# Kernel tuning notes

Measured on AMD Instinct MI355X. Metric: run time of the kernel, lower is better.

The kernel has to match this reference:

```python
import jax, jax.numpy as jnp
import numpy as np

N_HEADS = 16
ROPE_THETA = 10000.0


def _rope(x):
    # x: (b, h, t, d). Interleaved-pair rotary embedding (lucidrains
    # rotary_embedding_torch convention: rotate_half on (d r) pairs, r=2).
    b, h, t, d = x.shape
    inv_freq = 1.0 / (ROPE_THETA ** (jnp.arange(0, d, 2, dtype=jnp.float32) / d))  # (d/2,)
    ang = jnp.arange(t, dtype=jnp.float32)[:, None] * inv_freq[None, :]            # (t, d/2)
    cos = jnp.cos(ang)
    sin = jnp.sin(ang)
    xp = x.reshape(b, h, t, d // 2, 2)
    x1, x2 = xp[..., 0], xp[..., 1]
    o1 = x1 * cos - x2 * sin
    o2 = x1 * sin + x2 * cos
    return jnp.stack([o1, o2], axis=-1).reshape(b, h, t, d)


def setup_inputs() -> dict:
    key = jax.random.key(0)
    k1, k2, k3 = jax.random.split(key, 3)
    B, T, C = 4, 2048, 1024
    x = jax.random.normal(k1, (B, T, C), dtype=jnp.float32)
    # torch nn.Linear weight layout: (out_features, in_features)
    w_attn = jax.random.normal(k2, (3 * C, C), dtype=jnp.float32) * (1.0 / np.sqrt(C))
    w_proj = jax.random.normal(k3, (C, C), dtype=jnp.float32) * (1.0 / np.sqrt(C))
    return {"x": x, "w_attn": w_attn, "w_proj": w_proj}


def reference(x, w_attn, w_proj):
    B, T, C = x.shape
    H = N_HEADS
    D = C // H
    # fused QKV projection: (b, t, 3C)
    qkv = jnp.einsum('btc,fc->btf', x, w_attn)
    # rearrange 'b t (r h d) -> r b h t d'
    qkv = qkv.reshape(B, T, 3, H, D).transpose(2, 0, 3, 1, 4)
    q, k, v = qkv[0], qkv[1], qkv[2]
    q = _rope(q)
    k = _rope(k)
    scale = 1.0 / np.sqrt(D).astype(np.float32)
    scores = jnp.einsum('bhqd,bhkd->bhqk', q, k) * scale
    attn = jax.nn.softmax(scores, axis=-1)
    y = jnp.einsum('bhqk,bhkd->bhqd', attn, v)       # (b, h, t, d)
    y = y.transpose(0, 2, 1, 3).reshape(B, T, C)     # 'b h t d -> b t (h d)'
    return jnp.einsum('btc,oc->bto', y, w_proj)
```

## Files before the change

kernel.cpp:

```cpp
#include <hip/hip_runtime.h>
#include <hip/hip_bf16.h>
#include <math.h>

typedef __bf16 bf16;
typedef float f32x4 __attribute__((ext_vector_type(4)));
typedef float f32x16 __attribute__((ext_vector_type(16)));
typedef bf16 bf16x8 __attribute__((ext_vector_type(8)));
typedef bf16 bf16x4 __attribute__((ext_vector_type(4)));
typedef unsigned int uint;
typedef uint uintx2 __attribute__((ext_vector_type(2)));

#define MFMA16(a, b, c) __builtin_amdgcn_mfma_f32_16x16x32_bf16(a, b, c, 0, 0, 0)
#define MFMA32(a, b, c) __builtin_amdgcn_mfma_f32_32x32x16_bf16(a, b, c, 0, 0, 0)

static constexpr int T_SEQ = 2048;
static constexpr int CDIM  = 1024;
static constexpr int NH    = 16;
static constexpr int DH    = 64;
static constexpr float FREQ_C = 0.20762050593045998f;
static constexpr float Q_SCALE = 0.18033688011112042f;

__device__ __forceinline__ float fexp2(float x) {
    return __builtin_amdgcn_exp2f(x);
}

__device__ __forceinline__ uint pack_bf16(float lo, float hi) {
    union { bf16 h[2]; uint u; } cv;
    cv.h[0] = (bf16)lo;
    cv.h[1] = (bf16)hi;
    return cv.u;
}

__device__ __forceinline__ void gld_lds16(const bf16* g, bf16* l) {
    __builtin_amdgcn_global_load_lds(
        (const __attribute__((address_space(1))) void*)g,
        (__attribute__((address_space(3))) void*)l, 16, 0, 0);
}

__device__ __forceinline__ void fast_sincos(float x, float* s, float* c) {
    const float INV2PI = 0.15915494309189535f;
    const float PI2_HI = 6.28125f;
    const float PI2_LO = 1.9353071795864769e-3f;
    const float n = rintf(x * INV2PI);
    float r = fmaf(-n, PI2_HI, x);
    r = fmaf(-n, PI2_LO, r);
    *s = __sinf(r);
    *c = __cosf(r);
}

__global__ __launch_bounds__(256)
void rope_table(float2* __restrict__ tab) {
    const int i = blockIdx.x * 256 + threadIdx.x;
    const int t = i >> 5, p = i & 31;
    const float ang = (float)t * exp2f(-2.0f * (float)p * FREQ_C);
    float s, c;
    fast_sincos(ang, &s, &c);
    tab[i] = make_float2(c, s);
}

__global__ __launch_bounds__(256)
void cvt_f32_bf16(const float* __restrict__ in, bf16* __restrict__ out, int n8) {
    const int i = blockIdx.x * 256 + threadIdx.x;
    if (i >= n8) return;
    const f32x4* p = (const f32x4*)(in + (size_t)i * 8);
    const f32x4 lo = p[0], hi = p[1];
    bf16x8 o;
    o[0] = (bf16)lo[0]; o[1] = (bf16)lo[1]; o[2] = (bf16)lo[2]; o[3] = (bf16)lo[3];
    o[4] = (bf16)hi[0]; o[5] = (bf16)hi[1]; o[6] = (bf16)hi[2]; o[7] = (bf16)hi[3];
    *(bf16x8*)(out + (size_t)i * 8) = o;
}

#define GEMM_CORE(Abase, Bbase, KDIM)                                            \
    f32x4 acc[4][4] = {};                                                        \
    for (int kk = 0; kk < (KDIM); kk += 64) {                                    \
        __syncthreads();                                                         \
        _Pragma("unroll")                                                        \
        for (int u = 0; u < 4; u++) {                                            \
            const int st = wave * 4 + u, mg = st >> 1, kg = st & 1;              \
            gld_lds16(Abase + (size_t)(mg * 16 + sm) * (KDIM) + kk + kg * 32 + sc * 8, \
                      &ash[st * 512]);                                           \
            gld_lds16(Bbase + (size_t)(mg * 16 + sm) * (KDIM) + kk + kg * 32 + sc * 8, \
                      &bsh[st * 512]);                                           \
        }                                                                        \
        __syncthreads();                                                         \
        _Pragma("unroll")                                                        \
        for (int kg = 0; kg < 2; kg++) {                                         \
            bf16x8 af[4], bfr[4];                                                \
            _Pragma("unroll")                                                    \
            for (int a = 0; a < 4; a++)                                          \
                af[a] = *(const bf16x8*)&ash[((wm * 4 + a) * 2 + kg) * 512 + lane * 8]; \
            _Pragma("unroll")                                                    \
            for (int b = 0; b < 4; b++)                                          \
                bfr[b] = *(const bf16x8*)&bsh[((wn * 4 + b) * 2 + kg) * 512 + lane * 8]; \
            _Pragma("unroll")                                                    \
            for (int a = 0; a < 4; a++)                                          \
                _Pragma("unroll")                                                \
                for (int b = 0; b < 4; b++)                                      \
                    acc[a][b] = MFMA16(af[a], bfr[b], acc[a][b]);                \
        }                                                                        \
    }

__global__ __launch_bounds__(256)
void gemm_qkv(const bf16* __restrict__ X, const bf16* __restrict__ W,
              bf16* __restrict__ Qo, bf16* __restrict__ Ko, bf16* __restrict__ Vt,
              const float2* __restrict__ tab) {
    __shared__ __align__(16) bf16 ash[16 * 512];
    __shared__ __align__(16) bf16 bsh[16 * 512];
    const int tid = threadIdx.x, lane = tid & 63, wave = tid >> 6;
    const int quad = lane >> 4, l16 = lane & 15;
    const int wm = wave >> 1, wn = wave & 1;
    const int bm = blockIdx.y, bn = blockIdx.x;
    const int sm = lane & 15, sc = lane >> 4;

    const bf16* Abase = X + (size_t)(bm * 128) * CDIM;
    const bf16* Bbase = W + (size_t)(bn * 128) * CDIM;
    GEMM_CORE(Abase, Bbase, CDIM)

    const int rr    = (bn * 128) >> 10;
    const int nsec  = (bn * 128) & 1023;
    const int batch = (bm * 128) >> 11;
    const int tb    = ((bm * 128) & 2047) + wm * 64;

    if (rr == 2) {
#pragma unroll
        for (int b = 0; b < 4; b++) {
            const int n = nsec + wn * 64 + b * 16 + l16;
            const int h = n >> 6, d = n & 63;
            bf16* vp = Vt + ((size_t)(batch * NH + h) * DH + d) * T_SEQ;
#pragma unroll
            for (int a = 0; a < 4; a++) {
                const int t0 = tb + a * 16 + quad * 4;
                bf16x4 pk4 = { (bf16)acc[a][b][0], (bf16)acc[a][b][1],
                               (bf16)acc[a][b][2], (bf16)acc[a][b][3] };
                *(bf16x4*)(vp + t0) = pk4;
            }
        }
    } else {
        bf16* Dst = (rr == 0) ? Qo : Ko;
        const float scale = (rr == 0) ? Q_SCALE : 1.0f;
#pragma unroll
        for (int b = 0; b < 4; b++) {
            const int n = nsec + wn * 64 + b * 16 + l16;
            const int h = n >> 6, d = n & 63;
            const int p = d >> 1, odd = d & 1;
            bf16* dp = Dst + (size_t)(batch * NH + h) * T_SEQ * DH + d;
#pragma unroll
            for (int a = 0; a < 4; a++) {
#pragma unroll
                for (int r = 0; r < 4; r++) {
                    const int t = tb + a * 16 + quad * 4 + r;
                    const float val = acc[a][b][r];
                    const float partner = __shfl_xor(val, 1);
                    const float2 cs = tab[t * 32 + p];
                    float o = odd ? (partner * cs.y + val * cs.x)
                                  : (val * cs.x - partner * cs.y);
                    dp[(size_t)t * DH] = (bf16)(o * scale);
                }
            }
        }
    }
}

__global__ __launch_bounds__(256)
void gemm_proj(const bf16* __restrict__ X, const bf16* __restrict__ W,
               float* __restrict__ Out) {
    __shared__ __align__(16) bf16 ash[16 * 512];
    __shared__ __align__(16) bf16 bsh[16 * 512];
    const int tid = threadIdx.x, lane = tid & 63, wave = tid >> 6;
    const int quad = lane >> 4, l16 = lane & 15;
    const int wm = wave >> 1, wn = wave & 1;
    const int bm = blockIdx.y, bn = blockIdx.x;
    const int sm = lane & 15, sc = lane >> 4;

    const bf16* Abase = X + (size_t)(bm * 128) * CDIM;
    const bf16* Bbase = W + (size_t)(bn * 128) * CDIM;
    GEMM_CORE(Abase, Bbase, CDIM)

#pragma unroll
    for (int b = 0; b < 4; b++) {
        const int n = bn * 128 + wn * 64 + b * 16 + l16;
#pragma unroll
        for (int a = 0; a < 4; a++) {
            const int m = bm * 128 + wm * 64 + a * 16 + quad * 4;
#pragma unroll
            for (int r = 0; r < 4; r++)
                Out[(size_t)(m + r) * CDIM + n] = acc[a][b][r];
        }
    }
}

__global__ __launch_bounds__(256)
void flash(const bf16* __restrict__ Q, const bf16* __restrict__ K,
           const bf16* __restrict__ Vt, bf16* __restrict__ Y) {
    __shared__ __align__(16) bf16 ksh[2][8 * 512];
    __shared__ __align__(16) bf16 vsh[2][8 * 512];
    const int tid = threadIdx.x, lane = tid & 63, wave = tid >> 6;
    const int l32 = lane & 31, hi = lane >> 5;
    const int id = blockIdx.x;
    const int bh = (id & 7) * 8 + ((id >> 3) & 7);
    const int qb = id >> 6;
    const size_t kbase = (size_t)bh * T_SEQ * DH;
    const size_t vbase = (size_t)bh * DH * T_SEQ;
    const int q0 = qb * 128 + wave * 32;

    bf16x8 bq[4];
    const bf16* qp = Q + kbase + (size_t)(q0 + l32) * DH + hi * 8;
#pragma unroll
    for (int c = 0; c < 4; c++) bq[c] = *(const bf16x8*)(qp + c * 16);

    f32x16 oT[2] = {};
    f32x16 lf = {};
    bf16x8 onesf;
#pragma unroll
    for (int j = 0; j < 8; j++) onesf[j] = (bf16)1.0f;

#define STAGE(buf_, kt_) do {                                              \
        if (wave < 2) {                                                    \
            _Pragma("unroll")                                              \
            for (int u = 0; u < 4; u++) {                                  \
                const int s = wave * 4 + u, kb = s >> 2, c = s & 3;        \
                gld_lds16(K + kbase + (size_t)((kt_) + kb * 32 + l32) * DH \
                              + c * 16 + hi * 8,                           \
                          &ksh[buf_][s * 512]);                            \
            }                                                              \
        } else {                                                           \
            _Pragma("unroll")                                              \
            for (int u = 0; u < 4; u++) {                                  \
                const int s = (wave - 2) * 4 + u, db = s >> 2, kc = s & 3; \
                gld_lds16(Vt + vbase + (size_t)(db * 32 + l32) * T_SEQ     \
                              + (kt_) + kc * 16 + hi * 8,                  \
                          &vsh[buf_][s * 512]);                            \
            }                                                              \
        }                                                                  \
    } while (0)

    STAGE(0, 0);
    int ib = 0;
    for (int kt = 0; kt < T_SEQ; kt += 64, ib ^= 1) {
        __syncthreads();
        if (kt + 64 < T_SEQ) STAGE(ib ^ 1, kt + 64);

#pragma unroll
        for (int kb = 0; kb < 2; kb++) {
            f32x16 s = {};
#pragma unroll
            for (int c = 0; c < 4; c++) {
                const bf16x8 a = *(const bf16x8*)&ksh[ib][(kb * 4 + c) * 512 + lane * 8];
                s = MFMA32(a, bq[c], s);
            }
            uint P[8];
#pragma unroll
            for (int w = 0; w < 8; w++) {
                const float e0 = fexp2(s[2 * w]);
                const float e1 = fexp2(s[2 * w + 1]);
                P[w] = pack_bf16(e0, e1);
            }
#pragma unroll
            for (int t = 0; t < 2; t++) {
                const uintx2 rA = __builtin_amdgcn_permlane32_swap(
                    P[4 * t + 0], P[4 * t + 2], false, false);
                const uintx2 rB = __builtin_amdgcn_permlane32_swap(
                    P[4 * t + 1], P[4 * t + 3], false, false);
                union { uint u[4]; bf16x8 v; } bP;
                bP.u[0] = rA[0]; bP.u[1] = rB[0];
                bP.u[2] = rA[1]; bP.u[3] = rB[1];
                const int kc = kb * 2 + t;
                lf = MFMA32(onesf, bP.v, lf);
#pragma unroll
                for (int db = 0; db < 2; db++) {
                    const bf16x8 a = *(const bf16x8*)&vsh[ib][(db * 4 + kc) * 512 + lane * 8];
                    oT[db] = MFMA32(a, bP.v, oT[db]);
                }
            }
        }
    }
#undef STAGE

    const float inv = 1.0f / lf[0];

    const int b = bh >> 4, h = bh & 15;
    const size_t yrow = ((size_t)b * T_SEQ + q0 + l32) * CDIM + h * DH;
#pragma unroll
    for (int db = 0; db < 2; db++)
#pragma unroll
        for (int rg = 0; rg < 4; rg++) {
            bf16x4 o4 = { (bf16)(oT[db][rg * 4 + 0] * inv),
                          (bf16)(oT[db][rg * 4 + 1] * inv),
                          (bf16)(oT[db][rg * 4 + 2] * inv),
                          (bf16)(oT[db][rg * 4 + 3] * inv) };
            *(bf16x4*)(Y + yrow + db * 32 + 8 * rg + 4 * hi) = o4;
        }
}

extern "C" void kernel_launch(void* const* d_in, const int* in_sizes, int n_in,
                              void* d_out, int out_size, void* d_ws, size_t ws_size,
                              hipStream_t stream) {
    const float* x      = (const float*)d_in[0];
    const float* w_attn = (const float*)d_in[1];
    const float* w_proj = (const float*)d_in[2];
    float* out = (float*)d_out;

    bf16* ws = (bf16*)d_ws;
    const size_t SZ = (size_t)4 * NH * T_SEQ * DH;
    bf16* Xb  = ws;
    bf16* Wab = Xb + SZ;
    bf16* Wpb = Wab + 3145728;
    bf16* Qb  = Wpb + 1048576;
    bf16* Kb  = Qb + SZ;
    bf16* Vtb = Kb + SZ;
    bf16* Yb  = Vtb + SZ;
    float2* tab = (float2*)(Yb + SZ);

    rope_table<<<256, 256, 0, stream>>>(tab);
    cvt_f32_bf16<<<4096, 256, 0, stream>>>(x, Xb, 1048576);
    cvt_f32_bf16<<<1536, 256, 0, stream>>>(w_attn, Wab, 393216);
    cvt_f32_bf16<<<512, 256, 0, stream>>>(w_proj, Wpb, 131072);

    gemm_qkv<<<dim3(24, 64), 256, 0, stream>>>(Xb, Wab, Qb, Kb, Vtb, tab);
    flash<<<1024, 256, 0, stream>>>(Qb, Kb, Vtb, Yb);
    gemm_proj<<<dim3(8, 64), 256, 0, stream>>>(Yb, Wpb, out);
}
```

Baseline: 343.0 us.

## Process two query tiles per wave in flash kernel to reuse K/V loads

Each wave now handles two 32-row query tiles, 128 rows apart, so each block covers 256 queries and the grid is halved. Every K and V fragment read from shared memory is reused for both query tiles, which halves K/V global and LDS traffic per query. The cost is doubled accumulator registers, which may lower occupancy. With half as many blocks, the 256 CUs also get fewer waves to spread the work over.

```diff
diff --git a/kernel.cpp b/kernel.cpp
--- a/kernel.cpp
+++ b/kernel.cpp
@@ -198,18 +198,21 @@
     const int l32 = lane & 31, hi = lane >> 5;
     const int id = blockIdx.x;
     const int bh = (id & 7) * 8 + ((id >> 3) & 7);
-    const int qb = id >> 6;
+    const int qsb = id >> 6;
     const size_t kbase = (size_t)bh * T_SEQ * DH;
     const size_t vbase = (size_t)bh * DH * T_SEQ;
-    const int q0 = qb * 128 + wave * 32;
-
-    bf16x8 bq[4];
-    const bf16* qp = Q + kbase + (size_t)(q0 + l32) * DH + hi * 8;
-#pragma unroll
-    for (int c = 0; c < 4; c++) bq[c] = *(const bf16x8*)(qp + c * 16);
-
-    f32x16 oT[2] = {};
-    f32x16 lf = {};
+    const int q0 = qsb * 256 + wave * 32;
+
+    bf16x8 bq[2][4];
+#pragma unroll
+    for (int tq = 0; tq < 2; tq++) {
+        const bf16* qp = Q + kbase + (size_t)(q0 + tq * 128 + l32) * DH + hi * 8;
+#pragma unroll
+        for (int c = 0; c < 4; c++) bq[tq][c] = *(const bf16x8*)(qp + c * 16);
+    }
+
+    f32x16 oT[2][2] = {};
+    f32x16 lf[2] = {};
     bf16x8 onesf;
 #pragma unroll
     for (int j = 0; j < 8; j++) onesf[j] = (bf16)1.0f;
@@ -242,54 +245,62 @@
 
 #pragma unroll
         for (int kb = 0; kb < 2; kb++) {
-            f32x16 s = {};
+            f32x16 s0 = {}, s1 = {};
 #pragma unroll
             for (int c = 0; c < 4; c++) {
                 const bf16x8 a = *(const bf16x8*)&ksh[ib][(kb * 4 + c) * 512 + lane * 8];
-                s = MFMA32(a, bq[c], s);
-            }
-            uint P[8];
+                s0 = MFMA32(a, bq[0][c], s0);
+                s1 = MFMA32(a, bq[1][c], s1);
+            }
+            uint P[2][8];
 #pragma unroll
             for (int w = 0; w < 8; w++) {
-                const float e0 = fexp2(s[2 * w]);
-                const float e1 = fexp2(s[2 * w + 1]);
-                P[w] = pack_bf16(e0, e1);
+                P[0][w] = pack_bf16(fexp2(s0[2 * w]), fexp2(s0[2 * w + 1]));
+                P[1][w] = pack_bf16(fexp2(s1[2 * w]), fexp2(s1[2 * w + 1]));
             }
 #pragma unroll
             for (int t = 0; t < 2; t++) {
-                const uintx2 rA = __builtin_amdgcn_permlane32_swap(
-                    P[4 * t + 0], P[4 * t + 2], false, false);
-                const uintx2 rB = __builtin_amdgcn_permlane32_swap(
-                    P[4 * t + 1], P[4 * t + 3], false, false);
-                union { uint u[4]; bf16x8 v; } bP;
-                bP.u[0] = rA[0]; bP.u[1] = rB[0];
-                bP.u[2] = rA[1]; bP.u[3] = rB[1];
                 const int kc = kb * 2 + t;
-                lf = MFMA32(onesf, bP.v, lf);
-#pragma unroll
-                for (int db = 0; db < 2; db++) {
-                    const bf16x8 a = *(const bf16x8*)&vsh[ib][(db * 4 + kc) * 512 + lane * 8];
-                    oT[db] = MFMA32(a, bP.v, oT[db]);
+                bf16x8 vv[2];
+#pragma unroll
+                for (int db = 0; db < 2; db++)
+                    vv[db] = *(const bf16x8*)&vsh[ib][(db * 4 + kc) * 512 + lane * 8];
+#pragma unroll
+                for (int tq = 0; tq < 2; tq++) {
+                    const uintx2 rA = __builtin_amdgcn_permlane32_swap(
+                        P[tq][4 * t + 0], P[tq][4 * t + 2], false, false);
+                    const uintx2 rB = __builtin_amdgcn_permlane32_swap(
+                        P[tq][4 * t + 1], P[tq][4 * t + 3], false, false);
+                    union { uint u[4]; bf16x8 v; } bP;
+                    bP.u[0] = rA[0]; bP.u[1] = rB[0];
+                    bP.u[2] = rA[1]; bP.u[3] = rB[1];
+                    lf[tq] = MFMA32(onesf, bP.v, lf[tq]);
+#pragma unroll
+                    for (int db = 0; db < 2; db++)
+                        oT[tq][db] = MFMA32(vv[db], bP.v, oT[tq][db]);
                 }
             }
         }
     }
 #undef STAGE
 
-    const float inv = 1.0f / lf[0];
-
     const int b = bh >> 4, h = bh & 15;
-    const size_t yrow = ((size_t)b * T_SEQ + q0 + l32) * CDIM + h * DH;
-#pragma unroll
-    for (int db = 0; db < 2; db++)
-#pragma unroll
-        for (int rg = 0; rg < 4; rg++) {
-            bf16x4 o4 = { (bf16)(oT[db][rg * 4 + 0] * inv),
-                          (bf16)(oT[db][rg * 4 + 1] * inv),
-                          (bf16)(oT[db][rg * 4 + 2] * inv),
-                          (bf16)(oT[db][rg * 4 + 3] * inv) };
-            *(bf16x4*)(Y + yrow + db * 32 + 8 * rg + 4 * hi) = o4;
-        }
+#pragma unroll
+    for (int tq = 0; tq < 2; tq++) {
+        const float inv = 1.0f / lf[tq][0];
+        const size_t yrow =
+            ((size_t)b * T_SEQ + q0 + tq * 128 + l32) * CDIM + h * DH;
+#pragma unroll
+        for (int db = 0; db < 2; db++)
+#pragma unroll
+            for (int rg = 0; rg < 4; rg++) {
+                bf16x4 o4 = { (bf16)(oT[tq][db][rg * 4 + 0] * inv),
+                              (bf16)(oT[tq][db][rg * 4 + 1] * inv),
+                              (bf16)(oT[tq][db][rg * 4 + 2] * inv),
+                              (bf16)(oT[tq][db][rg * 4 + 3] * inv) };
+                *(bf16x4*)(Y + yrow + db * 32 + 8 * rg + 4 * hi) = o4;
+            }
+    }
 }
 
 extern "C" void kernel_launch(void* const* d_in, const int* in_sizes, int n_in,
@@ -317,6 +328,6 @@
     cvt_f32_bf16<<<512, 256, 0, stream>>>(w_proj, Wpb, 131072);
 
     gemm_qkv<<<dim3(24, 64), 256, 0, stream>>>(Xb, Wab, Qb, Kb, Vtb, tab);
-    flash<<<1024, 256, 0, stream>>>(Qb, Kb, Vtb, Yb);
+    flash<<<512, 256, 0, stream>>>(Qb, Kb, Vtb, Yb);
     gemm_proj<<<dim3(8, 64), 256, 0, stream>>>(Yb, Wpb, out);
 }
```

Result: faster. 329.4 us (-3.9%).
